# Kernel tuning notes

Hardware: AMD Instinct MI355X
Metric: run time of the kernel (lower is better)

## Reference

```python
import jax, jax.numpy as jnp
import numpy as np

C = 128


def _dw_conv(x, w, pad):
    # depthwise conv, NCHW, weight OIHW with I=1, groups=C
    return jax.lax.conv_general_dilated(
        x, w, window_strides=(1, 1), padding=pad,
        dimension_numbers=('NCHW', 'OIHW', 'NCHW'),
        feature_group_count=x.shape[1])


def _pw(x, w):
    # 1x1 conv as einsum; w: [O, I, 1, 1]
    return jnp.einsum('bihw,oi->bohw', x, w[:, :, 0, 0])


def _lrelu(x):
    return jax.nn.leaky_relu(x, 0.1)


def setup_inputs() -> dict:
    key = jax.random.key(0)
    ks = jax.random.split(key, 8)
    return {
        'x': jax.random.normal(ks[0], (2, C, 320, 320), dtype=jnp.float32),
        'w_h_dw': jax.random.normal(ks[1], (C, 1, 1, 5), dtype=jnp.float32) * 0.1,
        'w_h_pw': jax.random.normal(ks[2], (C, C, 1, 1), dtype=jnp.float32) * 0.05,
        'w_v_dw': jax.random.normal(ks[3], (C, 1, 5, 1), dtype=jnp.float32) * 0.1,
        'w_v_pw': jax.random.normal(ks[4], (C, C, 1, 1), dtype=jnp.float32) * 0.05,
        'w_dm1': jax.random.normal(ks[5], (C // 4, C, 1, 1), dtype=jnp.float32) * 0.05,
        'w_dm2': jax.random.normal(ks[6], (C, C // 4, 1, 1), dtype=jnp.float32) * 0.05,
        'w_fuse': jax.random.normal(ks[7], (C, 2 * C, 1, 1), dtype=jnp.float32) * 0.05,
        'scale': jnp.ones((1,), dtype=jnp.float32) * 0.3,
        'angRes': 5,
    }


def reference(x, w_h_dw, w_h_pw, w_v_dw, w_v_pw, w_dm1, w_dm2, w_fuse, scale, angRes):
    B, Cc, H, W = x.shape
    h, w = H // angRes, W // angRes
    # angular rearrange: [B,C,H,W] -> [B*h*w, C, angRes, angRes]
    xe = (x.reshape(B, Cc, h, angRes, w, angRes)
           .transpose(0, 2, 4, 1, 3, 5)
           .reshape(B * h * w, Cc, angRes, angRes))
    # horizontal EPI: depthwise 1x5 then 1x1
    eh = _pw(_lrelu(_dw_conv(xe, w_h_dw, ((0, 0), (2, 2)))), w_h_pw)
    # vertical EPI: depthwise 5x1 then 1x1
    ev = _pw(_lrelu(_dw_conv(xe, w_v_dw, ((2, 2), (0, 0)))), w_v_pw)

    def back(e):
        return (e.reshape(B, h, w, Cc, angRes, angRes)
                 .transpose(0, 3, 1, 4, 2, 5)
                 .reshape(B, Cc, H, W))

    eh, ev = back(eh), back(ev)
    epi = _pw(jnp.concatenate([eh, ev], axis=1), w_fuse)
    depth_w = jax.nn.sigmoid(_pw(_lrelu(_pw(epi, w_dm1)), w_dm2))
    return x + scale[0] * (epi * depth_w)
```

## Files before the change

kernel.cpp:

```cpp
#include <hip/hip_runtime.h>

typedef __bf16 bf16;
typedef __bf16 v8bf __attribute__((ext_vector_type(8)));
typedef __bf16 v4bf __attribute__((ext_vector_type(4)));
typedef float f32x4 __attribute__((ext_vector_type(4)));

#define MFMA16x16x32(a, b, c) __builtin_amdgcn_mfma_f32_16x16x32_bf16((a), (b), (c), 0, 0, 0)

__global__ void prep_wt(const float* __restrict__ wfuse,
                        const float* __restrict__ whpw,
                        const float* __restrict__ wvpw,
                        bf16* __restrict__ Wt) {
  int id = blockIdx.x * 256 + threadIdx.x;
  int o = id >> 8;
  int k = id & 255;
  const float* fr = wfuse + o * 256 + (k < 128 ? 0 : 128);
  const float* pw = (k < 128) ? whpw : wvpw;
  int ki = k & 127;
  float acc = 0.f;
#pragma unroll 8
  for (int j = 0; j < 128; ++j) acc = fmaf(fr[j], pw[j * 128 + ki], acc);
  Wt[o * 256 + k] = (bf16)acc;
}

__global__ void prep_dm(const float* __restrict__ wdm1,
                        const float* __restrict__ wdm2,
                        bf16* __restrict__ W1, bf16* __restrict__ W2) {
  int id = blockIdx.x * 256 + threadIdx.x;
  if (id < 4096) W1[id] = (bf16)wdm1[id];
  else           W2[id - 4096] = (bf16)wdm2[id - 4096];
}

__global__ __launch_bounds__(512, 2) void fused_main(
    const float* __restrict__ x,
    const float* __restrict__ whdw,
    const float* __restrict__ wvdw,
    const bf16* __restrict__ Wt,
    const bf16* __restrict__ W1,
    const bf16* __restrict__ W2,
    const float* __restrict__ scalep,
    float* __restrict__ out) {
  __shared__ float wdws[2][640];
  __shared__ __align__(16) char smem[57600];
  float* xs = (float*)smem;
  bf16* cs = (bf16*)(smem + 25600);

  const int tid = threadIdx.x;
  const int w = tid >> 6;
  const int lane = tid & 63;
  const int ln16 = lane & 15;
  const int q = lane >> 4;

  const int bx = blockIdx.x;
  const int wc = bx & 3;
  const int hi = (bx >> 2) & 63;
  const int b = bx >> 8;
  const int w0 = wc * 80;
  const size_t xbase = (size_t)b * 13107200 + (size_t)(hi * 5) * 320 + (size_t)w0;

  for (int i = tid; i < 1280; i += 512) {
    if (i < 640) wdws[0][i] = whdw[i];
    else         wdws[1][i - 640] = wvdw[i - 640];
  }

  f32x4 acc[4][8];
#pragma unroll
  for (int s = 0; s < 4; ++s)
#pragma unroll
    for (int m = 0; m < 8; ++m) acc[s][m] = (f32x4){0.f, 0.f, 0.f, 0.f};

  const int cpos = tid;
  int ca = 0, ccol = 0, caw = 0;
  if (cpos < 400) {
    ca = cpos / 80;
    ccol = cpos - ca * 80;
    caw = ccol % 5;
  }

  for (int kk = 0; kk < 8; ++kk) {
    const int c0 = kk * 16;
    __syncthreads();
    for (int i = tid; i < 1600; i += 512) {
      int c = i / 100;
      int rem = i - c * 100;
      int r = rem / 20;
      int c4 = rem - r * 20;
      const float4 v = *(const float4*)(x + xbase + (size_t)((c0 + c) * 102400 + r * 320 + c4 * 4));
      *(float4*)&xs[(c * 5 + r) * 80 + c4 * 4] = v;
    }
    __syncthreads();
    if (cpos < 400) {
#pragma unroll 4
      for (int c = 0; c < 16; ++c) {
        const float* xr = &xs[(c * 5 + ca) * 80];
        float dh = 0.f, dv = 0.f;
#pragma unroll
        for (int t = 0; t < 5; ++t) {
          const int d = t - 2;
          int okh = (unsigned)(caw + d) < 5u;
          int ih = ccol + d;
          ih = ih < 0 ? 0 : (ih > 79 ? 79 : ih);
          float vh = okh ? xr[ih] : 0.f;
          dh = fmaf(wdws[0][(c0 + c) * 5 + t], vh, dh);
          int okv = (unsigned)(ca + d) < 5u;
          int iv = ca + d;
          iv = iv < 0 ? 0 : (iv > 4 ? 4 : iv);
          float vv = okv ? xs[(c * 5 + iv) * 80 + ccol] : 0.f;
          dv = fmaf(wdws[1][(c0 + c) * 5 + t], vv, dv);
        }
        dh = fmaxf(dh, 0.f) + 0.1f * fminf(dh, 0.f);
        dv = fmaxf(dv, 0.f) + 0.1f * fminf(dv, 0.f);
        cs[cpos * 40 + c] = (bf16)dh;
        cs[cpos * 40 + 16 + c] = (bf16)dv;
      }
    }
    __syncthreads();
    v8bf af[8];
    const int koff = kk * 16 + (q & 1) * 8 + (q >> 1) * 128;
#pragma unroll
    for (int m = 0; m < 8; ++m)
      af[m] = *(const v8bf*)(Wt + (m * 16 + ln16) * 256 + koff);
#pragma unroll
    for (int s = 0; s < 4; ++s) {
      const int nt = w + 8 * s;
      if (nt < 25) {
        v8bf bfr = *(const v8bf*)(cs + (nt * 16 + ln16) * 40 + q * 8);
#pragma unroll
        for (int m = 0; m < 8; ++m) acc[s][m] = MFMA16x16x32(af[m], bfr, acc[s][m]);
      }
    }
  }
  __syncthreads();

  bf16* es = (bf16*)(smem + w * 4608);
  bf16* ts = (bf16*)(smem + 36864 + w * 1280);
  const float scl = scalep[0];

#pragma unroll
  for (int s = 0; s < 4; ++s) {
    const int nt = w + 8 * s;
    if (nt < 25) {
#pragma unroll
      for (int m = 0; m < 8; ++m) {
        v4bf v;
        v[0] = (bf16)acc[s][m][0];
        v[1] = (bf16)acc[s][m][1];
        v[2] = (bf16)acc[s][m][2];
        v[3] = (bf16)acc[s][m][3];
        *(v4bf*)(es + ln16 * 144 + m * 16 + q * 4) = v;
      }
      f32x4 tacc[2];
      tacc[0] = (f32x4){0.f, 0.f, 0.f, 0.f};
      tacc[1] = (f32x4){0.f, 0.f, 0.f, 0.f};
#pragma unroll
      for (int ks = 0; ks < 4; ++ks) {
        v8bf bfr = *(const v8bf*)(es + ln16 * 144 + ks * 32 + q * 8);
#pragma unroll
        for (int m2 = 0; m2 < 2; ++m2) {
          v8bf afr = *(const v8bf*)(W1 + (m2 * 16 + ln16) * 128 + ks * 32 + q * 8);
          tacc[m2] = MFMA16x16x32(afr, bfr, tacc[m2]);
        }
      }
#pragma unroll
      for (int m2 = 0; m2 < 2; ++m2) {
        v4bf v;
#pragma unroll
        for (int r = 0; r < 4; ++r) {
          float tv = tacc[m2][r];
          tv = fmaxf(tv, 0.f) + 0.1f * fminf(tv, 0.f);
          v[r] = (bf16)tv;
        }
        *(v4bf*)(ts + ln16 * 40 + m2 * 16 + q * 4) = v;
      }
      v8bf tb = *(const v8bf*)(ts + ln16 * 40 + q * 8);
      const int pos = nt * 16 + ln16;
      const int a = pos / 80;
      const int col = pos - a * 80;
      const size_t gb = xbase + (size_t)(a * 320 + col);
#pragma unroll
      for (int m = 0; m < 8; ++m) {
        v8bf afr2 = *(const v8bf*)(W2 + (m * 16 + ln16) * 32 + q * 8);
        f32x4 z = {0.f, 0.f, 0.f, 0.f};
        f32x4 dacc = MFMA16x16x32(afr2, tb, z);
#pragma unroll
        for (int r = 0; r < 4; ++r) {
          const int o = m * 16 + q * 4 + r;
          const float sig = 1.0f / (1.0f + __expf(-dacc[r]));
          const size_t g = gb + (size_t)o * 102400;
          out[g] = x[g] + scl * acc[s][m][r] * sig;
        }
      }
    }
  }
}

extern "C" void kernel_launch(void* const* d_in, const int* in_sizes, int n_in,
                              void* d_out, int out_size, void* d_ws, size_t ws_size,
                              hipStream_t stream) {
  (void)in_sizes; (void)n_in; (void)out_size; (void)ws_size;
  const float* x     = (const float*)d_in[0];
  const float* whdw  = (const float*)d_in[1];
  const float* whpw  = (const float*)d_in[2];
  const float* wvdw  = (const float*)d_in[3];
  const float* wvpw  = (const float*)d_in[4];
  const float* wdm1  = (const float*)d_in[5];
  const float* wdm2  = (const float*)d_in[6];
  const float* wfuse = (const float*)d_in[7];
  const float* scale = (const float*)d_in[8];

  bf16* Wt = (bf16*)d_ws;
  bf16* W1 = Wt + 32768;
  bf16* W2 = W1 + 4096;

  prep_wt<<<128, 256, 0, stream>>>(wfuse, whpw, wvpw, Wt);
  prep_dm<<<32, 256, 0, stream>>>(wdm1, wdm2, W1, W2);
  fused_main<<<512, 512, 0, stream>>>(x, whdw, wvdw, Wt, W1, W2, scale, (float*)d_out);
}
```

Baseline: 376.3 us.

## Double-buffer x tiles with async global-to-LDS loads and compute depthwise in MFMA fragments

The main kernel now stages each 16-channel x tile into LDS with global_load_lds async copies into two alternating buffers, prefetching the next tile while the current one is processed. The per-tile stage that wrote depthwise results into a shared bf16 buffer is gone: each lane computes the depthwise taps straight into its B-fragment registers, using precomputed tap indices and a zero pad slot, which removes two barriers per iteration. prep_wt is relaunched with 64-thread blocks and four independent accumulators. This trades more registers and some duplicated tap reads for less LDS traffic and fewer synchronisations.

```diff
diff --git a/kernel.cpp b/kernel.cpp
--- a/kernel.cpp
+++ b/kernel.cpp
@@ -1,4 +1,5 @@
 #include <hip/hip_runtime.h>
+#include <stdint.h>
 
 typedef __bf16 bf16;
 typedef __bf16 v8bf __attribute__((ext_vector_type(8)));
@@ -7,20 +8,29 @@
 
 #define MFMA16x16x32(a, b, c) __builtin_amdgcn_mfma_f32_16x16x32_bf16((a), (b), (c), 0, 0, 0)
 
-__global__ void prep_wt(const float* __restrict__ wfuse,
-                        const float* __restrict__ whpw,
-                        const float* __restrict__ wvpw,
-                        bf16* __restrict__ Wt) {
-  int id = blockIdx.x * 256 + threadIdx.x;
-  int o = id >> 8;
-  int k = id & 255;
+__device__ __forceinline__ void async_ld16(const float* g, float* l) {
+  __builtin_amdgcn_global_load_lds(
+      (const __attribute__((address_space(1))) uint32_t*)g,
+      (__attribute__((address_space(3))) uint32_t*)l, 16, 0, 0);
+}
+
+__global__ __launch_bounds__(64) void prep_wt(const float* __restrict__ wfuse,
+                                              const float* __restrict__ whpw,
+                                              const float* __restrict__ wvpw,
+                                              bf16* __restrict__ Wt) {
+  int id = blockIdx.x * 64 + threadIdx.x;
+  int o = id >> 8, k = id & 255, ki = k & 127;
   const float* fr = wfuse + o * 256 + (k < 128 ? 0 : 128);
   const float* pw = (k < 128) ? whpw : wvpw;
-  int ki = k & 127;
-  float acc = 0.f;
+  float a0 = 0.f, a1 = 0.f, a2 = 0.f, a3 = 0.f;
 #pragma unroll 8
-  for (int j = 0; j < 128; ++j) acc = fmaf(fr[j], pw[j * 128 + ki], acc);
-  Wt[o * 256 + k] = (bf16)acc;
+  for (int j = 0; j < 128; j += 4) {
+    a0 = fmaf(fr[j + 0], pw[(j + 0) * 128 + ki], a0);
+    a1 = fmaf(fr[j + 1], pw[(j + 1) * 128 + ki], a1);
+    a2 = fmaf(fr[j + 2], pw[(j + 2) * 128 + ki], a2);
+    a3 = fmaf(fr[j + 3], pw[(j + 3) * 128 + ki], a3);
+  }
+  Wt[o * 256 + k] = (bf16)((a0 + a1) + (a2 + a3));
 }
 
 __global__ void prep_dm(const float* __restrict__ wdm1,
@@ -40,28 +50,71 @@
     const bf16* __restrict__ W2,
     const float* __restrict__ scalep,
     float* __restrict__ out) {
-  __shared__ float wdws[2][640];
-  __shared__ __align__(16) char smem[57600];
-  float* xs = (float*)smem;
-  bf16* cs = (bf16*)(smem + 25600);
+  __shared__ __align__(16) char smemc[59904];
+  float* xs0 = (float*)smemc;
+  float* xs1 = (float*)(smemc + 25856);
+  float* whs = (float*)(smemc + 51712);
+  float* wvs = (float*)(smemc + 55808);
 
   const int tid = threadIdx.x;
-  const int w = tid >> 6;
-  const int lane = tid & 63;
-  const int ln16 = lane & 15;
-  const int q = lane >> 4;
+  const int w = tid >> 6, lane = tid & 63, ln16 = lane & 15, q = lane >> 4;
+  const int hv = q >> 1;
+  const int cb = (q & 1) * 8;
+  const bool has3 = (w == 0);
 
   const int bx = blockIdx.x;
-  const int wc = bx & 3;
-  const int hi = (bx >> 2) & 63;
-  const int b = bx >> 8;
-  const int w0 = wc * 80;
-  const size_t xbase = (size_t)b * 13107200 + (size_t)(hi * 5) * 320 + (size_t)w0;
+  const int wc = bx & 3, hi = (bx >> 2) & 63, b = bx >> 8;
+  const size_t xbase = (size_t)b * 13107200 + (size_t)(hi * 5) * 320 + (size_t)(wc * 80);
+  const float* gx = x + xbase;
 
   for (int i = tid; i < 1280; i += 512) {
-    if (i < 640) wdws[0][i] = whdw[i];
-    else         wdws[1][i - 640] = wvdw[i - 640];
-  }
+    int j = (i < 640) ? i : (i - 640);
+    int c = j / 5, t = j - c * 5;
+    float v = (i < 640) ? whdw[j] : wvdw[j];
+    ((i < 640) ? whs : wvs)[c * 8 + t] = v;
+  }
+  if (tid < 128) {
+    float* bufp = (tid & 64) ? xs1 : xs0;
+    int c = (tid & 63) >> 2, p = tid & 3;
+    bufp[c * 404 + 400 + p] = 0.f;
+  }
+
+  int ta[4][5];
+#pragma unroll
+  for (int s = 0; s < 4; ++s) {
+    int nt = w + 8 * s;
+    int pos = nt * 16 + ln16;
+    if (pos > 399) pos = 399;
+    int a = pos / 80;
+    int col = pos - a * 80;
+    int aw = col - (col / 5) * 5;
+#pragma unroll
+    for (int t = 0; t < 5; ++t) {
+      int d = t - 2;
+      int ah = ((unsigned)(aw + d) < 5u) ? (a * 80 + col + d) : 400;
+      int av = ((unsigned)(a + d) < 5u) ? ((a + d) * 80 + col) : 400;
+      ta[s][t] = hv ? av : ah;
+    }
+  }
+
+  auto stage = [&](int kk, float* buf) {
+    const int c0k = kk * 16;
+#pragma unroll
+    for (int h2 = 0; h2 < 2; ++h2) {
+      const int c = w + 8 * h2;
+      const float* gc = gx + (size_t)(c0k + c) * 102400;
+      float* lb = buf + c * 404;
+      {
+        int r = lane / 20, c4 = lane - r * 20;
+        async_ld16(gc + r * 320 + c4 * 4, lb);
+      }
+      if (lane < 36) {
+        int rem = 64 + lane;
+        int r = rem / 20, c4 = rem - r * 20;
+        async_ld16(gc + r * 320 + c4 * 4, lb + 256);
+      }
+    }
+  };
 
   f32x4 acc[4][8];
 #pragma unroll
@@ -69,71 +122,58 @@
 #pragma unroll
     for (int m = 0; m < 8; ++m) acc[s][m] = (f32x4){0.f, 0.f, 0.f, 0.f};
 
-  const int cpos = tid;
-  int ca = 0, ccol = 0, caw = 0;
-  if (cpos < 400) {
-    ca = cpos / 80;
-    ccol = cpos - ca * 80;
-    caw = ccol % 5;
-  }
+  stage(0, xs0);
 
   for (int kk = 0; kk < 8; ++kk) {
+    float* cur = (kk & 1) ? xs1 : xs0;
+    float* nxt = (kk & 1) ? xs0 : xs1;
     const int c0 = kk * 16;
     __syncthreads();
-    for (int i = tid; i < 1600; i += 512) {
-      int c = i / 100;
-      int rem = i - c * 100;
-      int r = rem / 20;
-      int c4 = rem - r * 20;
-      const float4 v = *(const float4*)(x + xbase + (size_t)((c0 + c) * 102400 + r * 320 + c4 * 4));
-      *(float4*)&xs[(c * 5 + r) * 80 + c4 * 4] = v;
-    }
-    __syncthreads();
-    if (cpos < 400) {
-#pragma unroll 4
-      for (int c = 0; c < 16; ++c) {
-        const float* xr = &xs[(c * 5 + ca) * 80];
-        float dh = 0.f, dv = 0.f;
-#pragma unroll
-        for (int t = 0; t < 5; ++t) {
-          const int d = t - 2;
-          int okh = (unsigned)(caw + d) < 5u;
-          int ih = ccol + d;
-          ih = ih < 0 ? 0 : (ih > 79 ? 79 : ih);
-          float vh = okh ? xr[ih] : 0.f;
-          dh = fmaf(wdws[0][(c0 + c) * 5 + t], vh, dh);
-          int okv = (unsigned)(ca + d) < 5u;
-          int iv = ca + d;
-          iv = iv < 0 ? 0 : (iv > 4 ? 4 : iv);
-          float vv = okv ? xs[(c * 5 + iv) * 80 + ccol] : 0.f;
-          dv = fmaf(wdws[1][(c0 + c) * 5 + t], vv, dv);
-        }
-        dh = fmaxf(dh, 0.f) + 0.1f * fminf(dh, 0.f);
-        dv = fmaxf(dv, 0.f) + 0.1f * fminf(dv, 0.f);
-        cs[cpos * 40 + c] = (bf16)dh;
-        cs[cpos * 40 + 16 + c] = (bf16)dv;
-      }
-    }
-    __syncthreads();
+
     v8bf af[8];
-    const int koff = kk * 16 + (q & 1) * 8 + (q >> 1) * 128;
+    const int koff = c0 + (q & 1) * 8 + hv * 128;
 #pragma unroll
     for (int m = 0; m < 8; ++m)
       af[m] = *(const v8bf*)(Wt + (m * 16 + ln16) * 256 + koff);
+
+    if (kk < 7) stage(kk + 1, nxt);
+
+    const float* wb8 = (hv ? wvs : whs) + (c0 + cb) * 8;
+    float frag[4][8];
+#pragma unroll
+    for (int c = 0; c < 8; ++c) {
+      const float4 wv4 = *(const float4*)(wb8 + c * 8);
+      const float w4v = wb8[c * 8 + 4];
+      const float* xp = cur + (cb + c) * 404;
+#pragma unroll
+      for (int s = 0; s < 4; ++s) {
+        if (s == 3 && !has3) continue;
+        float d = wv4.x * xp[ta[s][0]];
+        d = fmaf(wv4.y, xp[ta[s][1]], d);
+        d = fmaf(wv4.z, xp[ta[s][2]], d);
+        d = fmaf(wv4.w, xp[ta[s][3]], d);
+        frag[s][c] = fmaf(w4v, xp[ta[s][4]], d);
+      }
+    }
 #pragma unroll
     for (int s = 0; s < 4; ++s) {
-      const int nt = w + 8 * s;
-      if (nt < 25) {
-        v8bf bfr = *(const v8bf*)(cs + (nt * 16 + ln16) * 40 + q * 8);
-#pragma unroll
-        for (int m = 0; m < 8; ++m) acc[s][m] = MFMA16x16x32(af[m], bfr, acc[s][m]);
-      }
+      if (s == 3 && !has3) break;
+      v8bf bv;
+#pragma unroll
+      for (int c = 0; c < 8; ++c) {
+        float d = frag[s][c];
+        d = fmaxf(d, 0.f) + 0.1f * fminf(d, 0.f);
+        bv[c] = (bf16)d;
+      }
+#pragma unroll
+      for (int m = 0; m < 8; ++m)
+        acc[s][m] = MFMA16x16x32(af[m], bv, acc[s][m]);
     }
   }
   __syncthreads();
 
-  bf16* es = (bf16*)(smem + w * 4608);
-  bf16* ts = (bf16*)(smem + 36864 + w * 1280);
+  bf16* es = (bf16*)(smemc + w * 4608);
+  bf16* ts = (bf16*)(smemc + 36864 + w * 1280);
   const float scl = scalep[0];
 
 #pragma unroll
@@ -212,7 +252,7 @@
   bf16* W1 = Wt + 32768;
   bf16* W2 = W1 + 4096;
 
-  prep_wt<<<128, 256, 0, stream>>>(wfuse, whpw, wvpw, Wt);
+  prep_wt<<<512, 64, 0, stream>>>(wfuse, whpw, wvpw, Wt);
   prep_dm<<<32, 256, 0, stream>>>(wdm1, wdm2, W1, W2);
   fused_main<<<512, 512, 0, stream>>>(x, whdw, wvdw, Wt, W1, W2, scale, (float*)d_out);
 }
```

Result: slower. 587.2 us (+56.0%).
